# Kernel tuning notes

Measured on AMD Instinct MI355X. Metric: run time of the kernel, lower is better.

Reference implementation:

```python
import jax, jax.numpy as jnp
import numpy as np

N, D = 8192, 256
NEG_BIG = -9e15


def setup_inputs() -> dict:
    key = jax.random.key(0)
    k1, k2, k3 = jax.random.split(key, 3)
    h = jax.random.normal(k1, (N, D), dtype=jnp.float32)
    adj = jax.random.randint(k2, (N, N), 0, 2, dtype=jnp.int32)
    # xavier_uniform for a of shape (2D, 1): bound = sqrt(6/(2D+1))
    bound = np.sqrt(6.0 / (2 * D + 1)).astype(np.float32)
    a = jax.random.uniform(k3, (2 * D, 1), dtype=jnp.float32, minval=-bound, maxval=bound)
    return {"h": h, "adj": adj, "a": a}


def reference(h, adj, a):
    d = h.shape[1]
    h1 = h @ a[:d]            # [N, 1]
    h2 = h @ a[d:]            # [N, 1]
    e = jax.nn.leaky_relu(h1 + h2.T, negative_slope=0.01)  # [N, N]
    attention = jnp.where(adj > 0, e, NEG_BIG)
    attention = jax.nn.softmax(attention, axis=1)
    # dropout skipped: eval mode (training=False)
    return attention @ h      # [N, D]
```

## Files before the change

kernel.cpp:

```cpp
#include <hip/hip_runtime.h>
#include <hip/hip_bf16.h>

#define NTOT 8192
#define DDIM 256
#define ROWS 32
#define JSPL 2
#define JHALF (NTOT / JSPL)
#define NBATCH 64
#define NTSTR 131584
#define HTF_ELEMS (16 * NTSTR)
#define PSTR 40

typedef __attribute__((ext_vector_type(8))) short short8;
typedef __attribute__((ext_vector_type(4))) short short4v;
typedef __attribute__((ext_vector_type(4))) float floatx4;
typedef __attribute__((ext_vector_type(4))) int intx4;

static __device__ __forceinline__ short bfp(float f) {
  __hip_bfloat16 b = __float2bfloat16(f);
  return *(short*)&b;
}

__global__ __launch_bounds__(256) void gat_scores(const float* __restrict__ h,
                                                  const float* __restrict__ a,
                                                  float4* __restrict__ rc,
                                                  float2* __restrict__ etab) {
  int row  = blockIdx.x * 4 + (threadIdx.x >> 6);
  int lane = threadIdx.x & 63;
  const float* hr = h + (size_t)row * DDIM;
  float p1 = 0.f, p2 = 0.f;
#pragma unroll
  for (int k = 0; k < DDIM / 64; ++k) {
    int idx  = lane + 64 * k;
    float hv = hr[idx];
    p1 += hv * a[idx];
    p2 += hv * a[DDIM + idx];
  }
#pragma unroll
  for (int off = 32; off > 0; off >>= 1) {
    p1 += __shfl_down(p1, off, 64);
    p2 += __shfl_down(p2, off, 64);
  }
  if (lane == 0) {
    rc[row]   = make_float4(__expf(p1), __expf(0.01f * p1), 0.f, 0.f);
    etab[row] = make_float2(__expf(p2), __expf(0.01f * p2));
  }
}

__global__ __launch_bounds__(256) void gat_hpack(const float* __restrict__ h,
                                                 ushort* __restrict__ hTf) {
  __shared__ float tile[64][257];
  const int t    = threadIdx.x;
  const int lane = t & 63;
  const int w    = t >> 6;
  const int quad = lane >> 4;
  const int c    = lane & 15;
  const int i0   = blockIdx.x * 64;

#pragma unroll
  for (int it = 0; it < 16; ++it) {
    int r = it * 4 + w;
    float4 v = *(const float4*)(h + (size_t)(i0 + r) * DDIM + lane * 4);
    tile[r][lane * 4 + 0] = v.x; tile[r][lane * 4 + 1] = v.y;
    tile[r][lane * 4 + 2] = v.z; tile[r][lane * 4 + 3] = v.w;
  }
  __syncthreads();

#pragma unroll
  for (int k = 0; k < 4; ++k) {
    const int n = 4 * k + w;
#pragma unroll
    for (int jbl = 0; jbl < 2; ++jbl) {
      short8 vv;
#pragma unroll
      for (int i = 0; i < 8; ++i) {
        float f = tile[jbl * 32 + quad * 8 + i][n * 16 + c];
        vv[i] = bfp(f);
      }
      *(short8*)(hTf + ((size_t)(n * 257 + i0 / 32 + jbl) * 64 + lane) * 8) = vv;
    }
  }
}

__global__ __launch_bounds__(512, 4) void gat_attn(const ushort* __restrict__ hTf,
                                                   const int* __restrict__ adj,
                                                   const float4* __restrict__ rc,
                                                   const float2* __restrict__ etab,
                                                   float* __restrict__ pout,
                                                   float* __restrict__ plp) {
  __shared__ __align__(16) ushort Pb[2][2][32 * PSTR];
  __shared__ float lsum[8][32];

  const int t    = threadIdx.x;
  const int lane = t & 63;
  const int w    = t >> 6;
  const int quad = lane >> 4;
  const int c    = lane & 15;
  const int r0   = blockIdx.x * ROWS;
  const int jb   = blockIdx.y;

  const int brow  = lane & 31;
  const int btile = w & 1;
  const int bjo   = ((w >> 1) * 2 + (lane >> 5)) * 4;
  const float4 rcv = rc[r0 + brow];
  const float E1 = rcv.x, E2 = rcv.y;

  const int*   abase = adj + (size_t)(r0 + brow) * NTOT + (size_t)jb * JHALF + btile * 32 + bjo;
  const float* ebase = (const float*)(etab + (size_t)jb * JHALF + btile * 32 + bjo);
  const ushort* hbase = hTf + (size_t)(2 * w) * NTSTR + ((size_t)(jb * 128) * 64 + lane) * 8;

  floatx4 acc[2][2];
#pragma unroll
  for (int rt = 0; rt < 2; ++rt)
#pragma unroll
    for (int nn = 0; nn < 2; ++nn) acc[rt][nn] = (floatx4){0.f, 0.f, 0.f, 0.f};

  float lps = 0.f, lpdead = 0.f;
  intx4  ajs[2];
  float4 es[2][2];
  short8 bD[2][4];

  #define LDAE(S, bp)                                                          \
    ajs[S]   = __builtin_nontemporal_load((const intx4*)(abase + (bp) * 64));  \
    es[S][0] = *(const float4*)(ebase + (bp) * 128);                           \
    es[S][1] = *(const float4*)(ebase + (bp) * 128 + 4);

  #define LDB(S, bp)                                                           \
    bD[S][0] = *(const short8*)(hbase + (size_t)((bp) * 2 + 0) * 512);         \
    bD[S][1] = *(const short8*)(hbase + NTSTR + (size_t)((bp) * 2 + 0) * 512); \
    bD[S][2] = *(const short8*)(hbase + (size_t)((bp) * 2 + 1) * 512);         \
    bD[S][3] = *(const short8*)(hbase + NTSTR + (size_t)((bp) * 2 + 1) * 512);

  #define BUILD(S, LACC)                                                       \
    {                                                                          \
      short4v pk; float p;                                                     \
      p = (ajs[S][0] > 0) ? fmaxf(E1 * es[S][0].x, E2 * es[S][0].y) : 0.f; LACC += p; pk[0] = bfp(p); \
      p = (ajs[S][1] > 0) ? fmaxf(E1 * es[S][0].z, E2 * es[S][0].w) : 0.f; LACC += p; pk[1] = bfp(p); \
      p = (ajs[S][2] > 0) ? fmaxf(E1 * es[S][1].x, E2 * es[S][1].y) : 0.f; LACC += p; pk[2] = bfp(p); \
      p = (ajs[S][3] > 0) ? fmaxf(E1 * es[S][1].z, E2 * es[S][1].w) : 0.f; LACC += p; pk[3] = bfp(p); \
      *(short4v*)&Pb[S][btile][brow * PSTR + bjo] = pk;                        \
    }

  LDAE(0, 0)
  LDAE(1, 1)
  LDB(0, 0)
  LDB(1, 1)
  BUILD(0, lpdead)
  __syncthreads();

  #define ITER(bt, CUR, NXT)                                                   \
    {                                                                          \
      short8 pa00 = *(const short8*)&Pb[CUR][0][c * PSTR + quad * 8];          \
      short8 pa01 = *(const short8*)&Pb[CUR][0][(16 + c) * PSTR + quad * 8];   \
      short8 pa10 = *(const short8*)&Pb[CUR][1][c * PSTR + quad * 8];          \
      short8 pa11 = *(const short8*)&Pb[CUR][1][(16 + c) * PSTR + quad * 8];   \
      BUILD(NXT, lps)                                                          \
      {                                                                        \
        const int bp = ((bt) + 2) & (NBATCH - 1);                              \
        LDAE(CUR, bp)                                                          \
      }                                                                        \
      acc[0][0] = __builtin_amdgcn_mfma_f32_16x16x32_bf16(pa00, bD[CUR][0], acc[0][0], 0, 0, 0); \
      acc[0][1] = __builtin_amdgcn_mfma_f32_16x16x32_bf16(pa00, bD[CUR][1], acc[0][1], 0, 0, 0); \
      acc[1][0] = __builtin_amdgcn_mfma_f32_16x16x32_bf16(pa01, bD[CUR][0], acc[1][0], 0, 0, 0); \
      acc[1][1] = __builtin_amdgcn_mfma_f32_16x16x32_bf16(pa01, bD[CUR][1], acc[1][1], 0, 0, 0); \
      acc[0][0] = __builtin_amdgcn_mfma_f32_16x16x32_bf16(pa10, bD[CUR][2], acc[0][0], 0, 0, 0); \
      acc[0][1] = __builtin_amdgcn_mfma_f32_16x16x32_bf16(pa10, bD[CUR][3], acc[0][1], 0, 0, 0); \
      acc[1][0] = __builtin_amdgcn_mfma_f32_16x16x32_bf16(pa11, bD[CUR][2], acc[1][0], 0, 0, 0); \
      acc[1][1] = __builtin_amdgcn_mfma_f32_16x16x32_bf16(pa11, bD[CUR][3], acc[1][1], 0, 0, 0); \
      {                                                                        \
        const int bp = ((bt) + 2) & (NBATCH - 1);                              \
        LDB(CUR, bp)                                                           \
      }                                                                        \
      __syncthreads();                                                         \
    }

  for (int tt = 0; tt < NBATCH; tt += 2) {
    ITER(tt, 0, 1)
    ITER(tt + 1, 1, 0)
  }
  #undef ITER
  #undef BUILD
  #undef LDB
  #undef LDAE

  lps += __shfl_xor(lps, 32, 64);
  if (lane < 32) lsum[w][lane] = lps;
  __syncthreads();
  if (w == 0 && lane < 32) {
    float s = 0.f;
#pragma unroll
    for (int wi = 0; wi < 8; ++wi) s += lsum[wi][lane];
    plp[(size_t)jb * NTOT + r0 + lane] = s;
  }

  float* pob = pout + (size_t)jb * NTOT * DDIM;
#pragma unroll
  for (int rt = 0; rt < 2; ++rt)
#pragma unroll
    for (int nn = 0; nn < 2; ++nn)
#pragma unroll
      for (int reg = 0; reg < 4; ++reg)
        pob[(size_t)(r0 + rt * 16 + quad * 4 + reg) * DDIM + w * 32 + nn * 16 + c] =
            acc[rt][nn][reg];
}

__global__ __launch_bounds__(256) void gat_combine(const float* __restrict__ pout,
                                                   const float* __restrict__ plp,
                                                   float* __restrict__ out) {
  const int idx = blockIdx.x * 256 + threadIdx.x;
  const int row = idx >> 6;
  float4 a = ((const float4*)pout)[idx];
  float4 b = ((const float4*)(pout + (size_t)NTOT * DDIM))[idx];
  float inv = 1.f / (plp[row] + plp[NTOT + row]);
  float4 r;
  r.x = (a.x + b.x) * inv;
  r.y = (a.y + b.y) * inv;
  r.z = (a.z + b.z) * inv;
  r.w = (a.w + b.w) * inv;
  __builtin_nontemporal_store(r.x, &((float*)out)[idx * 4 + 0]);
  __builtin_nontemporal_store(r.y, &((float*)out)[idx * 4 + 1]);
  __builtin_nontemporal_store(r.z, &((float*)out)[idx * 4 + 2]);
  __builtin_nontemporal_store(r.w, &((float*)out)[idx * 4 + 3]);
}

extern "C" void kernel_launch(void* const* d_in, const int* in_sizes, int n_in,
                              void* d_out, int out_size, void* d_ws, size_t ws_size,
                              hipStream_t stream) {
  const float* h   = (const float*)d_in[0];
  const int*   adj = (const int*)d_in[1];
  const float* a   = (const float*)d_in[2];
  float* out = (float*)d_out;

  float4*   rc    = (float4*)d_ws;
  float2*   etab  = (float2*)(rc + NTOT);
  ushort*   hTf   = (ushort*)(etab + NTOT);
  float*    pout  = (float*)(hTf + HTF_ELEMS);
  float*    plp   = pout + (size_t)JSPL * NTOT * DDIM;

  gat_scores<<<NTOT / 4, 256, 0, stream>>>(h, a, rc, etab);
  gat_hpack<<<NTOT / 64, 256, 0, stream>>>(h, hTf);
  gat_attn<<<dim3(NTOT / ROWS, JSPL), 512, 0, stream>>>(hTf, adj, rc, etab, pout, plp);
  gat_combine<<<(NTOT * DDIM / 4) / 256, 256, 0, stream>>>(pout, plp, out);
}
```

Baseline: 467.0 us.

## Build P directly in MFMA registers, drop LDS staging and per-iteration barriers

Restructures the attention kernel so each wave computes its own bf16 probability fragment in registers (16 rows per block, waves split columns and j-range) and feeds it straight into MFMA. This removes the shared-memory P buffer and the barrier on every iteration. Exp is now computed per element from the raw scores instead of the precomputed factorised exp products, which adds transcendental work. The two j-halves are reduced through LDS at the end. h tiles are now reused across only 16 rows instead of 32, which roughly doubles hTf reads.

```diff
diff --git a/kernel.cpp b/kernel.cpp
--- a/kernel.cpp
+++ b/kernel.cpp
@@ -3,16 +3,15 @@
 
 #define NTOT 8192
 #define DDIM 256
-#define ROWS 32
+#define RTILE 16
 #define JSPL 2
-#define JHALF (NTOT / JSPL)
-#define NBATCH 64
+#define JBLK (NTOT / JSPL)
+#define JWAVE (JBLK / 2)
+#define NITER (JWAVE / 32)
 #define NTSTR 131584
 #define HTF_ELEMS (16 * NTSTR)
-#define PSTR 40
 
 typedef __attribute__((ext_vector_type(8))) short short8;
-typedef __attribute__((ext_vector_type(4))) short short4v;
 typedef __attribute__((ext_vector_type(4))) float floatx4;
 typedef __attribute__((ext_vector_type(4))) int intx4;
 
@@ -23,8 +22,8 @@
 
 __global__ __launch_bounds__(256) void gat_scores(const float* __restrict__ h,
                                                   const float* __restrict__ a,
-                                                  float4* __restrict__ rc,
-                                                  float2* __restrict__ etab) {
+                                                  float* __restrict__ s1,
+                                                  float* __restrict__ s2) {
   int row  = blockIdx.x * 4 + (threadIdx.x >> 6);
   int lane = threadIdx.x & 63;
   const float* hr = h + (size_t)row * DDIM;
@@ -41,10 +40,7 @@
     p1 += __shfl_down(p1, off, 64);
     p2 += __shfl_down(p2, off, 64);
   }
-  if (lane == 0) {
-    rc[row]   = make_float4(__expf(p1), __expf(0.01f * p1), 0.f, 0.f);
-    etab[row] = make_float2(__expf(p2), __expf(0.01f * p2));
-  }
+  if (lane == 0) { s1[row] = p1; s2[row] = p2; }
 }
 
 __global__ __launch_bounds__(256) void gat_hpack(const float* __restrict__ h,
@@ -82,126 +78,120 @@
   }
 }
 
-__global__ __launch_bounds__(512, 4) void gat_attn(const ushort* __restrict__ hTf,
+__global__ __launch_bounds__(256, 4) void gat_attn(const ushort* __restrict__ hTf,
                                                    const int* __restrict__ adj,
-                                                   const float4* __restrict__ rc,
-                                                   const float2* __restrict__ etab,
+                                                   const float* __restrict__ s1,
+                                                   const float* __restrict__ s2,
                                                    float* __restrict__ pout,
                                                    float* __restrict__ plp) {
-  __shared__ __align__(16) ushort Pb[2][2][32 * PSTR];
-  __shared__ float lsum[8][32];
+  __shared__ float slab[2][32][64];
+  __shared__ float lpred[2][16];
 
   const int t    = threadIdx.x;
   const int lane = t & 63;
   const int w    = t >> 6;
   const int quad = lane >> 4;
   const int c    = lane & 15;
-  const int r0   = blockIdx.x * ROWS;
+  const int ch   = w & 1;
+  const int jc   = w >> 1;
+  const int r0   = blockIdx.x * RTILE;
   const int jb   = blockIdx.y;
-
-  const int brow  = lane & 31;
-  const int btile = w & 1;
-  const int bjo   = ((w >> 1) * 2 + (lane >> 5)) * 4;
-  const float4 rcv = rc[r0 + brow];
-  const float E1 = rcv.x, E2 = rcv.y;
-
-  const int*   abase = adj + (size_t)(r0 + brow) * NTOT + (size_t)jb * JHALF + btile * 32 + bjo;
-  const float* ebase = (const float*)(etab + (size_t)jb * JHALF + btile * 32 + bjo);
-  const ushort* hbase = hTf + (size_t)(2 * w) * NTSTR + ((size_t)(jb * 128) * 64 + lane) * 8;
-
-  floatx4 acc[2][2];
-#pragma unroll
-  for (int rt = 0; rt < 2; ++rt)
-#pragma unroll
-    for (int nn = 0; nn < 2; ++nn) acc[rt][nn] = (floatx4){0.f, 0.f, 0.f, 0.f};
-
-  float lps = 0.f, lpdead = 0.f;
-  intx4  ajs[2];
-  float4 es[2][2];
-  short8 bD[2][4];
-
-  #define LDAE(S, bp)                                                          \
-    ajs[S]   = __builtin_nontemporal_load((const intx4*)(abase + (bp) * 64));  \
-    es[S][0] = *(const float4*)(ebase + (bp) * 128);                           \
-    es[S][1] = *(const float4*)(ebase + (bp) * 128 + 4);
-
-  #define LDB(S, bp)                                                           \
-    bD[S][0] = *(const short8*)(hbase + (size_t)((bp) * 2 + 0) * 512);         \
-    bD[S][1] = *(const short8*)(hbase + NTSTR + (size_t)((bp) * 2 + 0) * 512); \
-    bD[S][2] = *(const short8*)(hbase + (size_t)((bp) * 2 + 1) * 512);         \
-    bD[S][3] = *(const short8*)(hbase + NTSTR + (size_t)((bp) * 2 + 1) * 512);
-
-  #define BUILD(S, LACC)                                                       \
+  const int j0   = jb * JBLK + jc * JWAVE;
+
+  const float a1 = s1[r0 + c];
+
+  const int*    ap = adj + (size_t)(r0 + c) * NTOT + j0 + quad * 8;
+  const float*  sp = s2 + j0 + quad * 8;
+  const ushort* hb = hTf + (size_t)(ch * 8) * NTSTR + ((size_t)(j0 / 32) * 64 + lane) * 8;
+
+  floatx4 acc[8];
+#pragma unroll
+  for (int q = 0; q < 8; ++q) acc[q] = (floatx4){0.f, 0.f, 0.f, 0.f};
+
+  float lp = 0.f;
+  short8 bA[4], bB[4];
+  intx4  aj0, aj1;
+  float4 sv0, sv1;
+
+  #define LDA(jt)                                                              \
     {                                                                          \
-      short4v pk; float p;                                                     \
-      p = (ajs[S][0] > 0) ? fmaxf(E1 * es[S][0].x, E2 * es[S][0].y) : 0.f; LACC += p; pk[0] = bfp(p); \
-      p = (ajs[S][1] > 0) ? fmaxf(E1 * es[S][0].z, E2 * es[S][0].w) : 0.f; LACC += p; pk[1] = bfp(p); \
-      p = (ajs[S][2] > 0) ? fmaxf(E1 * es[S][1].x, E2 * es[S][1].y) : 0.f; LACC += p; pk[2] = bfp(p); \
-      p = (ajs[S][3] > 0) ? fmaxf(E1 * es[S][1].z, E2 * es[S][1].w) : 0.f; LACC += p; pk[3] = bfp(p); \
-      *(short4v*)&Pb[S][btile][brow * PSTR + bjo] = pk;                        \
+      const int* p_ = ap + (size_t)(jt) * 32;                                  \
+      aj0 = __builtin_nontemporal_load((const intx4*)p_);                      \
+      aj1 = __builtin_nontemporal_load((const intx4*)(p_ + 4));                \
+      sv0 = *(const float4*)(sp + (jt) * 32);                                  \
+      sv1 = *(const float4*)(sp + (jt) * 32 + 4);                              \
     }
-
-  LDAE(0, 0)
-  LDAE(1, 1)
-  LDB(0, 0)
-  LDB(1, 1)
-  BUILD(0, lpdead)
+  #define LDBA(jt)                                                             \
+    _Pragma("unroll")                                                          \
+    for (int q = 0; q < 4; ++q)                                                \
+      bA[q] = *(const short8*)(hb + (size_t)(jt) * 512 + (size_t)q * NTSTR);
+  #define LDBB(jt)                                                             \
+    _Pragma("unroll")                                                          \
+    for (int q = 0; q < 4; ++q)                                                \
+      bB[q] = *(const short8*)(hb + (size_t)(jt) * 512 + (size_t)(4 + q) * NTSTR);
+
+  LDBA(0)
+  LDBB(0)
+  LDA(0)
+
+  for (int jt = 0; jt < NITER; ++jt) {
+    const int jn = (jt + 1) & (NITER - 1);
+
+    const float sarr[8] = {sv0.x, sv0.y, sv0.z, sv0.w, sv1.x, sv1.y, sv1.z, sv1.w};
+    const int   aarr[8] = {aj0[0], aj0[1], aj0[2], aj0[3], aj1[0], aj1[1], aj1[2], aj1[3]};
+    short8 pa;
+#pragma unroll
+    for (int i = 0; i < 8; ++i) {
+      const float e  = a1 + sarr[i];
+      const float l  = fmaxf(e, 0.01f * e);
+      const float pe = __expf(l);
+      const float p  = (aarr[i] > 0) ? pe : 0.f;
+      lp += p;
+      pa[i] = bfp(p);
+    }
+
+    LDA(jn)
+
+#pragma unroll
+    for (int q = 0; q < 4; ++q)
+      acc[q] = __builtin_amdgcn_mfma_f32_16x16x32_bf16(pa, bA[q], acc[q], 0, 0, 0);
+    LDBA(jn)
+
+#pragma unroll
+    for (int q = 0; q < 4; ++q)
+      acc[4 + q] = __builtin_amdgcn_mfma_f32_16x16x32_bf16(pa, bB[q], acc[4 + q], 0, 0, 0);
+    LDBB(jn)
+  }
+  #undef LDA
+  #undef LDBA
+  #undef LDBB
+
+  lp += __shfl_xor(lp, 16, 64);
+  lp += __shfl_xor(lp, 32, 64);
+
+  if (jc == 1) {
+#pragma unroll
+    for (int q = 0; q < 8; ++q)
+#pragma unroll
+      for (int r = 0; r < 4; ++r) slab[ch][q * 4 + r][lane] = acc[q][r];
+    if (lane < 16) lpred[ch][lane] = lp;
+  }
   __syncthreads();
-
-  #define ITER(bt, CUR, NXT)                                                   \
-    {                                                                          \
-      short8 pa00 = *(const short8*)&Pb[CUR][0][c * PSTR + quad * 8];          \
-      short8 pa01 = *(const short8*)&Pb[CUR][0][(16 + c) * PSTR + quad * 8];   \
-      short8 pa10 = *(const short8*)&Pb[CUR][1][c * PSTR + quad * 8];          \
-      short8 pa11 = *(const short8*)&Pb[CUR][1][(16 + c) * PSTR + quad * 8];   \
-      BUILD(NXT, lps)                                                          \
-      {                                                                        \
-        const int bp = ((bt) + 2) & (NBATCH - 1);                              \
-        LDAE(CUR, bp)                                                          \
-      }                                                                        \
-      acc[0][0] = __builtin_amdgcn_mfma_f32_16x16x32_bf16(pa00, bD[CUR][0], acc[0][0], 0, 0, 0); \
-      acc[0][1] = __builtin_amdgcn_mfma_f32_16x16x32_bf16(pa00, bD[CUR][1], acc[0][1], 0, 0, 0); \
-      acc[1][0] = __builtin_amdgcn_mfma_f32_16x16x32_bf16(pa01, bD[CUR][0], acc[1][0], 0, 0, 0); \
-      acc[1][1] = __builtin_amdgcn_mfma_f32_16x16x32_bf16(pa01, bD[CUR][1], acc[1][1], 0, 0, 0); \
-      acc[0][0] = __builtin_amdgcn_mfma_f32_16x16x32_bf16(pa10, bD[CUR][2], acc[0][0], 0, 0, 0); \
-      acc[0][1] = __builtin_amdgcn_mfma_f32_16x16x32_bf16(pa10, bD[CUR][3], acc[0][1], 0, 0, 0); \
-      acc[1][0] = __builtin_amdgcn_mfma_f32_16x16x32_bf16(pa11, bD[CUR][2], acc[1][0], 0, 0, 0); \
-      acc[1][1] = __builtin_amdgcn_mfma_f32_16x16x32_bf16(pa11, bD[CUR][3], acc[1][1], 0, 0, 0); \
-      {                                                                        \
-        const int bp = ((bt) + 2) & (NBATCH - 1);                              \
-        LDB(CUR, bp)                                                           \
-      }                                                                        \
-      __syncthreads();                                                         \
-    }
-
-  for (int tt = 0; tt < NBATCH; tt += 2) {
-    ITER(tt, 0, 1)
-    ITER(tt + 1, 1, 0)
-  }
-  #undef ITER
-  #undef BUILD
-  #undef LDB
-  #undef LDAE
-
-  lps += __shfl_xor(lps, 32, 64);
-  if (lane < 32) lsum[w][lane] = lps;
-  __syncthreads();
-  if (w == 0 && lane < 32) {
-    float s = 0.f;
-#pragma unroll
-    for (int wi = 0; wi < 8; ++wi) s += lsum[wi][lane];
-    plp[(size_t)jb * NTOT + r0 + lane] = s;
-  }
-
-  float* pob = pout + (size_t)jb * NTOT * DDIM;
-#pragma unroll
-  for (int rt = 0; rt < 2; ++rt)
-#pragma unroll
-    for (int nn = 0; nn < 2; ++nn)
-#pragma unroll
-      for (int reg = 0; reg < 4; ++reg)
-        pob[(size_t)(r0 + rt * 16 + quad * 4 + reg) * DDIM + w * 32 + nn * 16 + c] =
-            acc[rt][nn][reg];
+  if (jc == 0) {
+#pragma unroll
+    for (int q = 0; q < 8; ++q)
+#pragma unroll
+      for (int r = 0; r < 4; ++r) acc[q][r] += slab[ch][q * 4 + r][lane];
+    lp += lpred[ch][c];
+
+    float* pob = pout + (size_t)jb * NTOT * DDIM;
+#pragma unroll
+    for (int q = 0; q < 8; ++q)
+#pragma unroll
+      for (int r = 0; r < 4; ++r)
+        pob[(size_t)(r0 + quad * 4 + r) * DDIM + ch * 128 + q * 16 + c] = acc[q][r];
+    if (ch == 0 && quad == 0) plp[(size_t)jb * NTOT + r0 + c] = lp;
+  }
 }
 
 __global__ __launch_bounds__(256) void gat_combine(const float* __restrict__ pout,
@@ -231,14 +221,14 @@
   const float* a   = (const float*)d_in[2];
   float* out = (float*)d_out;
 
-  float4*   rc    = (float4*)d_ws;
-  float2*   etab  = (float2*)(rc + NTOT);
-  ushort*   hTf   = (ushort*)(etab + NTOT);
+  float*    s1    = (float*)d_ws;
+  float*    s2    = s1 + NTOT;
+  ushort*   hTf   = (ushort*)(s2 + NTOT);
   float*    pout  = (float*)(hTf + HTF_ELEMS);
   float*    plp   = pout + (size_t)JSPL * NTOT * DDIM;
 
-  gat_scores<<<NTOT / 4, 256, 0, stream>>>(h, a, rc, etab);
+  gat_scores<<<NTOT / 4, 256, 0, stream>>>(h, a, s1, s2);
   gat_hpack<<<NTOT / 64, 256, 0, stream>>>(h, hTf);
-  gat_attn<<<dim3(NTOT / ROWS, JSPL), 512, 0, stream>>>(hTf, adj, rc, etab, pout, plp);
+  gat_attn<<<dim3(NTOT / RTILE, JSPL), 256, 0, stream>>>(hTf, adj, s1, s2, pout, plp);
   gat_combine<<<(NTOT * DDIM / 4) / 256, 256, 0, stream>>>(pout, plp, out);
 }
```

Result: slower. 520.9 us (+11.6%).
